# Performance work log

Hardware: AMD Instinct MI355X
Metric: run time of the kernel (lower is better)

Reference implementation:

```python
import jax, jax.numpy as jnp
import numpy as np

WSCALE = 0.05  # keep qk logits in a stable range for softmax

def setup_inputs() -> dict:
    key = jax.random.key(0)
    ks = jax.random.split(key, 7)
    B, C, H, W = 8, 256, 64, 64
    d = C // 8
    x = jax.random.normal(ks[0], (B, C, H, W), dtype=jnp.float32)
    Wq = jax.random.normal(ks[1], (d, C), dtype=jnp.float32) * WSCALE
    Wk = jax.random.normal(ks[2], (d, C), dtype=jnp.float32) * WSCALE
    Wv = jax.random.normal(ks[3], (C, C), dtype=jnp.float32) * WSCALE
    bq = jnp.zeros((d,), jnp.float32)
    bk = jnp.zeros((d,), jnp.float32)
    bv = jnp.zeros((C,), jnp.float32)
    return {"x": x, "Wq": Wq, "bq": bq, "Wk": Wk, "bk": bk, "Wv": Wv, "bv": bv}

def reference(x, Wq, bq, Wk, bk, Wv, bv):
    B, C, H, W = x.shape
    N = H * W
    xf = x.reshape(B, C, N)                                  # [B,C,N]
    # 1x1 convs == per-pixel linear projections
    q = jnp.einsum('dc,bcn->bdn', Wq, xf) + bq[None, :, None]  # [B,d,N]
    k = jnp.einsum('dc,bcn->bdn', Wk, xf) + bk[None, :, None]  # [B,d,N]
    v = jnp.einsum('ec,bcn->ben', Wv, xf) + bv[None, :, None]  # [B,C,N]
    # attn[b,i,j] = q_i . k_j ; softmax over j (keys)
    attn = jax.nn.softmax(jnp.einsum('bdi,bdj->bij', q, k), axis=-1)  # [B,N,N]
    # out[b,c,i] = sum_j v[b,c,j] * attn[b,i,j]
    out = jnp.einsum('bcj,bij->bci', v, attn)                # [B,C,N]
    return out.reshape(B, C, H, W)
```

## Files before the change

kernel.cpp:

```cpp
#include <hip/hip_runtime.h>
#include <math.h>

#define NB 8
#define NC 256
#define ND 32
#define NN 4096
#define NM 320
#define LOG2E 1.44269504088896f
#define XSTR 264

typedef short short8 __attribute__((ext_vector_type(8)));
typedef float f32x4 __attribute__((ext_vector_type(4)));

#define LDS_BARRIER() asm volatile("s_waitcnt lgkmcnt(0)\ns_barrier" ::: "memory")

__device__ __forceinline__ unsigned int f2bf_u(float f) {
    return (__float_as_uint(f) + 0x8000u) >> 16;
}
__device__ __forceinline__ unsigned short f2bf(float f) {
    return (unsigned short)f2bf_u(f);
}

__global__ __launch_bounds__(256) void repack_kernel(
    const float* __restrict__ Wq, const float* __restrict__ bq,
    const float* __restrict__ Wk, const float* __restrict__ bk,
    const float* __restrict__ Wv, const float* __restrict__ bv,
    unsigned short* __restrict__ wp, float* __restrict__ bias)
{
    const int T    = blockIdx.x * 256 + threadIdx.x;
    const int j    = T & 7;
    const int lane = (T >> 3) & 63;
    const int ks   = (T >> 9) & 7;
    const int mt   = T >> 12;
    const int m = mt * 16 + (lane & 15);
    const int k = ks * 32 + ((lane >> 4) << 3) + j;
    float wv;
    if (m < 32)       wv = Wq[m * NC + k] * LOG2E;
    else if (m < 64)  wv = Wk[(m - 32) * NC + k];
    else              wv = Wv[(m - 64) * NC + k];
    wp[T] = f2bf(wv);
    if (T < NM) {
        float bb;
        if (T < 32)      bb = bq[T] * LOG2E;
        else if (T < 64) bb = bk[T - 32];
        else             bb = bv[T - 64];
        bias[T] = bb;
    }
}

__global__ __launch_bounds__(256, 4) void proj_kernel(
    const float* __restrict__ x,
    const unsigned short* __restrict__ wp,
    const float* __restrict__ bias,
    unsigned short* __restrict__ q_ws,
    unsigned short* __restrict__ k_ws,
    unsigned short* __restrict__ v_ws)
{
    __shared__ __align__(16) unsigned short xs[32 * XSTR];

    const int b  = blockIdx.x >> 7;
    const int n0 = (blockIdx.x & 127) << 5;
    const int t  = threadIdx.x;

    {
        const int n  = t & 31;
        const int cg = t >> 5;
        const float* xb = x + (size_t)b * NC * NN + n0 + n;
        #pragma unroll
        for (int it = 0; it < 8; ++it) {
            const int c = 32 * it + 4 * cg;
            const float x0 = xb[(size_t)(c + 0) * NN];
            const float x1 = xb[(size_t)(c + 1) * NN];
            const float x2 = xb[(size_t)(c + 2) * NN];
            const float x3 = xb[(size_t)(c + 3) * NN];
            uint2 pk;
            pk.x = (f2bf_u(x1) << 16) | f2bf_u(x0);
            pk.y = (f2bf_u(x3) << 16) | f2bf_u(x2);
            *(uint2*)(xs + n * XSTR + c) = pk;
        }
    }
    __syncthreads();

    const int w    = t >> 6;
    const int lane = t & 63;
    const int li = lane & 15;
    const int qd = lane >> 4;

    f32x4 acc[5][2];
    #pragma unroll
    for (int u = 0; u < 5; ++u) {
        const float bb = bias[(w + 4 * u) * 16 + li];
        acc[u][0] = (f32x4){bb, bb, bb, bb};
        acc[u][1] = (f32x4){bb, bb, bb, bb};
    }

    #pragma unroll
    for (int ks = 0; ks < 8; ++ks) {
        short8 af[2];
        #pragma unroll
        for (int mt = 0; mt < 2; ++mt)
            af[mt] = *(const short8*)(xs + (mt * 16 + li) * XSTR + ks * 32 + qd * 8);
        #pragma unroll
        for (int u = 0; u < 5; ++u) {
            const int ct = w + 4 * u;
            const short8 bf = *(const short8*)(wp + (size_t)((ct * 8 + ks) * 64 + lane) * 8);
            acc[u][0] = __builtin_amdgcn_mfma_f32_16x16x32_bf16(af[0], bf, acc[u][0], 0, 0, 0);
            acc[u][1] = __builtin_amdgcn_mfma_f32_16x16x32_bf16(af[1], bf, acc[u][1], 0, 0, 0);
        }
    }

    #pragma unroll
    for (int u = 0; u < 5; ++u) {
        const int ct = w + 4 * u;
        if (ct < 4) {
            unsigned short* dst = (ct < 2) ? q_ws : k_ws;
            const int d = (ct & 1) * 16 + li;
            #pragma unroll
            for (int mt = 0; mt < 2; ++mt)
                #pragma unroll
                for (int r = 0; r < 4; ++r) {
                    const int n = n0 + mt * 16 + 4 * qd + r;
                    dst[((size_t)b * NN + n) * ND + d] = f2bf(acc[u][mt][r]);
                }
        } else {
            const int cv = (ct - 4) * 16 + li;
            #pragma unroll
            for (int mt = 0; mt < 2; ++mt) {
                const int n = n0 + mt * 16 + 4 * qd;
                uint2 pk;
                pk.x = (f2bf_u(acc[u][mt][1]) << 16) | f2bf_u(acc[u][mt][0]);
                pk.y = (f2bf_u(acc[u][mt][3]) << 16) | f2bf_u(acc[u][mt][2]);
                *(uint2*)(v_ws + ((size_t)b * NC + cv) * NN + n) = pk;
            }
        }
    }
}

__global__ __launch_bounds__(256, 2) void attn_kernel(
    const unsigned short* __restrict__ q_ws,
    const unsigned short* __restrict__ k_ws,
    const unsigned short* __restrict__ v_ws,
    float* __restrict__ out)
{
    __shared__ __align__(16) unsigned short Pb[2][4][16 * 72];
    __shared__ float lred[4][16];

    const int b  = blockIdx.x & 7;
    const int i0 = (blockIdx.x >> 3) * 64;
    const int w    = threadIdx.x >> 6;
    const int lane = threadIdx.x & 63;
    const int li = lane & 15;
    const int qd = lane >> 4;
    const int sw = w;
    const int c0 = 64 * w;

    const short8 qf = *(const short8*)(q_ws + ((size_t)b * NN + i0 + 16 * sw + li) * ND + qd * 8);
    const unsigned short* kb = k_ws + ((size_t)b * NN + li) * ND + qd * 8;
    const unsigned short* vb = v_ws + ((size_t)b * NC + c0 + li) * NN + qd * 8;

    unsigned short* PA = &Pb[0][0][0];
    unsigned short* PB = &Pb[1][0][0];

    f32x4 o[4][4];
    #pragma unroll
    for (int sb = 0; sb < 4; ++sb)
        #pragma unroll
        for (int ct = 0; ct < 4; ++ct)
            o[sb][ct] = (f32x4){0.f, 0.f, 0.f, 0.f};
    float l_loc = 0.f;
    const f32x4 z4 = {0.f, 0.f, 0.f, 0.f};

    short8 kA[4], kB[4], vA[4][2], vB[4][2];

    auto LKF = [&](int j0, short8 (&kf)[4]) {
        #pragma unroll
        for (int tt = 0; tt < 4; ++tt)
            kf[tt] = *(const short8*)(kb + (size_t)(j0 + 16 * tt) * ND);
    };
    auto LVF = [&](int j0, short8 (&vf)[4][2]) {
        #pragma unroll
        for (int t = 0; t < 4; ++t) {
            const unsigned short* vt = vb + (size_t)(16 * t) * NN;
            vf[t][0] = *(const short8*)(vt + j0);
            vf[t][1] = *(const short8*)(vt + j0 + 32);
        }
    };
    auto DOS = [&](short8 (&kf)[4], unsigned short* P) {
        unsigned short* Pw = P + sw * (16 * 72) + li * 72 + 4 * qd;
        #pragma unroll
        for (int tt = 0; tt < 4; ++tt) {
            const f32x4 s = __builtin_amdgcn_mfma_f32_16x16x32_bf16(kf[tt], qf, z4, 0, 0, 0);
            const float p0 = __builtin_amdgcn_exp2f(s[0]);
            const float p1 = __builtin_amdgcn_exp2f(s[1]);
            const float p2 = __builtin_amdgcn_exp2f(s[2]);
            const float p3 = __builtin_amdgcn_exp2f(s[3]);
            l_loc += (p0 + p1) + (p2 + p3);
            const unsigned u0 = __float_as_uint(p0) + 0x8000u;
            const unsigned u1 = __float_as_uint(p1) + 0x8000u;
            const unsigned u2 = __float_as_uint(p2) + 0x8000u;
            const unsigned u3 = __float_as_uint(p3) + 0x8000u;
            uint2 pk;
            pk.x = __builtin_amdgcn_perm(u1, u0, 0x07060302u);
            pk.y = __builtin_amdgcn_perm(u3, u2, 0x07060302u);
            *(uint2*)(Pw + 16 * tt) = pk;
        }
    };
    auto DOPV = [&](const unsigned short* P, short8 (&vf)[4][2]) {
        #pragma unroll
        for (int sb = 0; sb < 4; ++sb) {
            const unsigned short* Pr = P + sb * (16 * 72) + li * 72 + qd * 8;
            const short8 pf0 = *(const short8*)(Pr);
            const short8 pf1 = *(const short8*)(Pr + 32);
            #pragma unroll
            for (int ct = 0; ct < 4; ++ct) {
                o[sb][ct] = __builtin_amdgcn_mfma_f32_16x16x32_bf16(vf[ct][0], pf0, o[sb][ct], 0, 0, 0);
                o[sb][ct] = __builtin_amdgcn_mfma_f32_16x16x32_bf16(vf[ct][1], pf1, o[sb][ct], 0, 0, 0);
            }
        }
    };

    LKF(0, kA); LVF(0, vA);
    DOS(kA, PA);
    LKF(64, kB);
    LDS_BARRIER();

    int j = 0;
    #pragma unroll 1
    for (int it = 0; it < 31; ++it) {
        LVF(j + 64, vB);
        DOS(kB, PB);
        DOPV(PA, vA);
        LKF(j + 128, kA);
        LDS_BARRIER();
        LVF(j + 128, vA);
        DOS(kA, PA);
        DOPV(PB, vB);
        LKF(j + 192, kB);
        LDS_BARRIER();
        j += 128;
    }
    LVF(4032, vB);
    DOS(kB, PB);
    DOPV(PA, vA);
    LDS_BARRIER();
    DOPV(PB, vB);

    l_loc += __shfl_xor(l_loc, 16, 64);
    l_loc += __shfl_xor(l_loc, 32, 64);
    if (lane < 16) lred[w][li] = l_loc;
    __syncthreads();
    float linv[4];
    #pragma unroll
    for (int sb = 0; sb < 4; ++sb)
        linv[sb] = 1.0f / lred[sb][li];

    #pragma unroll
    for (int sb = 0; sb < 4; ++sb)
        #pragma unroll
        for (int ct = 0; ct < 4; ++ct) {
            const int c = c0 + ct * 16 + qd * 4;
            float* op = out + ((size_t)b * NC + c) * NN + i0 + 16 * sb + li;
            #pragma unroll
            for (int r = 0; r < 4; ++r)
                op[(size_t)r * NN] = o[sb][ct][r] * linv[sb];
        }
}

extern "C" void kernel_launch(void* const* d_in, const int* in_sizes, int n_in,
                              void* d_out, int out_size, void* d_ws, size_t ws_size,
                              hipStream_t stream) {
    const float* x  = (const float*)d_in[0];
    const float* Wq = (const float*)d_in[1];
    const float* bq = (const float*)d_in[2];
    const float* Wk = (const float*)d_in[3];
    const float* bk = (const float*)d_in[4];
    const float* Wv = (const float*)d_in[5];
    const float* bv = (const float*)d_in[6];
    float* out = (float*)d_out;

    unsigned short* q_ws = (unsigned short*)d_ws;
    unsigned short* k_ws = q_ws + (size_t)NB * NN * ND;
    unsigned short* v_ws = k_ws + (size_t)NB * NN * ND;
    unsigned short* wp   = v_ws + (size_t)NB * NC * NN;
    float*          bias = (float*)(wp + (size_t)NM * NC);

    repack_kernel<<<NM * NC / 256, 256, 0, stream>>>(Wq, bq, Wk, bk, Wv, bv, wp, bias);
    proj_kernel<<<NB * (NN / 32), 256, 0, stream>>>(x, wp, bias, q_ws, k_ws, v_ws);
    attn_kernel<<<NB * (NN / 64), 256, 0, stream>>>(q_ws, k_ws, v_ws, out);
}
```

Baseline: 252.3 us.

## Quad-buffer P tiles in LDS to halve barriers in attention loop

Grows the shared P (softmax probability) buffer from two to four tiles and reorganises the pipelined loop so each barrier covers two key/value blocks instead of one. Loop trip count halves (15 iterations of 256 keys) and the prologue/epilogue are rewritten to match. The goal is to cut workgroup barrier stalls and give more slack between the score and PV MFMA phases. It doubles the P LDS footprint, which may lower occupancy, and it changes the register live ranges.

Result: no change. 247.4 us (-1.9%).

```diff
diff --git a/kernel.cpp b/kernel.cpp
--- a/kernel.cpp
+++ b/kernel.cpp
@@ -142,7 +142,7 @@
     const unsigned short* __restrict__ v_ws,
     float* __restrict__ out)
 {
-    __shared__ __align__(16) unsigned short Pb[2][4][16 * 72];
+    __shared__ __align__(16) unsigned short Pb[4][4][16 * 72];
     __shared__ float lred[4][16];
 
     const int b  = blockIdx.x & 7;
@@ -158,8 +158,10 @@
     const unsigned short* kb = k_ws + ((size_t)b * NN + li) * ND + qd * 8;
     const unsigned short* vb = v_ws + ((size_t)b * NC + c0 + li) * NN + qd * 8;
 
-    unsigned short* PA = &Pb[0][0][0];
-    unsigned short* PB = &Pb[1][0][0];
+    unsigned short* Pq0 = &Pb[0][0][0];
+    unsigned short* Pq1 = &Pb[1][0][0];
+    unsigned short* Pq2 = &Pb[2][0][0];
+    unsigned short* Pq3 = &Pb[3][0][0];
 
     f32x4 o[4][4];
     #pragma unroll
@@ -219,31 +221,46 @@
         }
     };
 
-    LKF(0, kA); LVF(0, vA);
-    DOS(kA, PA);
-    LKF(64, kB);
+    LKF(0, kA); LKF(64, kB); LVF(0, vA);
+    DOS(kA, Pq0);
+    DOS(kB, Pq1);
+    LKF(128, kA);
     LDS_BARRIER();
 
     int j = 0;
     #pragma unroll 1
-    for (int it = 0; it < 31; ++it) {
+    for (int it = 0; it < 15; ++it) {
         LVF(j + 64, vB);
-        DOS(kB, PB);
-        DOPV(PA, vA);
-        LKF(j + 128, kA);
+        DOPV(Pq0, vA);
+        DOS(kA, Pq2);
+        LKF(j + 192, kB);
+        LVF(j + 128, vA);
+        DOPV(Pq1, vB);
+        DOS(kB, Pq3);
+        LKF(j + 256, kA);
         LDS_BARRIER();
-        LVF(j + 128, vA);
-        DOS(kA, PA);
-        DOPV(PB, vB);
-        LKF(j + 192, kB);
+        LVF(j + 192, vB);
+        DOPV(Pq2, vA);
+        DOS(kA, Pq0);
+        LKF(j + 320, kB);
+        LVF(j + 256, vA);
+        DOPV(Pq3, vB);
+        DOS(kB, Pq1);
+        LKF(j + 384, kA);
         LDS_BARRIER();
-        j += 128;
-    }
+        j += 256;
+    }
+    LVF(3904, vB);
+    DOPV(Pq0, vA);
+    DOS(kA, Pq2);
+    LKF(4032, kB);
+    LVF(3968, vA);
+    DOPV(Pq1, vB);
+    DOS(kB, Pq3);
+    LDS_BARRIER();
     LVF(4032, vB);
-    DOS(kB, PB);
-    DOPV(PA, vA);
-    LDS_BARRIER();
-    DOPV(PB, vB);
+    DOPV(Pq2, vA);
+    DOPV(Pq3, vB);
 
     l_loc += __shfl_xor(l_loc, 16, 64);
     l_loc += __shfl_xor(l_loc, 32, 64);
```

## Keep attention probabilities in registers and drop LDS exchange between waves

Applied to the files above, without the earlier changes.

Each wave now computes the scores for all four 16-row query sub-blocks itself instead of sharing them through LDS. The bf16 probabilities feed straight from the QK MFMA output layout into 16x16x16 PV MFMAs, so the LDS buffers and per-chunk barriers go away. This costs 4x redundant QK MFMAs and exp2 work per wave, plus smaller 8-byte V loads and twice as many PV MFMA instructions. Sched barriers pin the order of loads and compute.

New measurement: 588.0 us. 133% more time.

```diff
diff --git a/kernel.cpp b/kernel.cpp
--- a/kernel.cpp
+++ b/kernel.cpp
@@ -10,9 +10,8 @@
 #define XSTR 264
 
 typedef short short8 __attribute__((ext_vector_type(8)));
+typedef short short4v __attribute__((ext_vector_type(4)));
 typedef float f32x4 __attribute__((ext_vector_type(4)));
-
-#define LDS_BARRIER() asm volatile("s_waitcnt lgkmcnt(0)\ns_barrier" ::: "memory")
 
 __device__ __forceinline__ unsigned int f2bf_u(float f) {
     return (__float_as_uint(f) + 0x8000u) >> 16;
@@ -142,24 +141,24 @@
     const unsigned short* __restrict__ v_ws,
     float* __restrict__ out)
 {
-    __shared__ __align__(16) unsigned short Pb[2][4][16 * 72];
-    __shared__ float lred[4][16];
-
     const int b  = blockIdx.x & 7;
     const int i0 = (blockIdx.x >> 3) * 64;
     const int w    = threadIdx.x >> 6;
     const int lane = threadIdx.x & 63;
     const int li = lane & 15;
     const int qd = lane >> 4;
-    const int sw = w;
     const int c0 = 64 * w;
 
-    const short8 qf = *(const short8*)(q_ws + ((size_t)b * NN + i0 + 16 * sw + li) * ND + qd * 8);
+    short8 qf[4];
+    #pragma unroll
+    for (int sb = 0; sb < 4; ++sb)
+        qf[sb] = *(const short8*)(q_ws + ((size_t)b * NN + i0 + 16 * sb + li) * ND + qd * 8);
+
     const unsigned short* kb = k_ws + ((size_t)b * NN + li) * ND + qd * 8;
-    const unsigned short* vb = v_ws + ((size_t)b * NC + c0 + li) * NN + qd * 8;
-
-    unsigned short* PA = &Pb[0][0][0];
-    unsigned short* PB = &Pb[1][0][0];
+    const unsigned short* vrow[4];
+    #pragma unroll
+    for (int ct = 0; ct < 4; ++ct)
+        vrow[ct] = v_ws + ((size_t)b * NC + c0 + 16 * ct + li) * NN + qd * 4;
 
     f32x4 o[4][4];
     #pragma unroll
@@ -167,103 +166,88 @@
         #pragma unroll
         for (int ct = 0; ct < 4; ++ct)
             o[sb][ct] = (f32x4){0.f, 0.f, 0.f, 0.f};
-    float l_loc = 0.f;
+    float l_loc[4] = {0.f, 0.f, 0.f, 0.f};
     const f32x4 z4 = {0.f, 0.f, 0.f, 0.f};
 
-    short8 kA[4], kB[4], vA[4][2], vB[4][2];
-
-    auto LKF = [&](int j0, short8 (&kf)[4]) {
-        #pragma unroll
-        for (int tt = 0; tt < 4; ++tt)
-            kf[tt] = *(const short8*)(kb + (size_t)(j0 + 16 * tt) * ND);
+    short8 kA[4], kB[4];
+    uint2  vA[4][4], vB[4][4];
+
+    auto LK = [&](int j0, short8 (&kf)[4]) {
+        #pragma unroll
+        for (int jt = 0; jt < 4; ++jt)
+            kf[jt] = *(const short8*)(kb + (size_t)(j0 + 16 * jt) * ND);
     };
-    auto LVF = [&](int j0, short8 (&vf)[4][2]) {
-        #pragma unroll
-        for (int t = 0; t < 4; ++t) {
-            const unsigned short* vt = vb + (size_t)(16 * t) * NN;
-            vf[t][0] = *(const short8*)(vt + j0);
-            vf[t][1] = *(const short8*)(vt + j0 + 32);
-        }
+    auto LV = [&](int j0, uint2 (&vf)[4][4]) {
+        #pragma unroll
+        for (int ct = 0; ct < 4; ++ct)
+            #pragma unroll
+            for (int jt = 0; jt < 4; ++jt)
+                vf[ct][jt] = *(const uint2*)(vrow[ct] + j0 + 16 * jt);
     };
-    auto DOS = [&](short8 (&kf)[4], unsigned short* P) {
-        unsigned short* Pw = P + sw * (16 * 72) + li * 72 + 4 * qd;
-        #pragma unroll
-        for (int tt = 0; tt < 4; ++tt) {
-            const f32x4 s = __builtin_amdgcn_mfma_f32_16x16x32_bf16(kf[tt], qf, z4, 0, 0, 0);
-            const float p0 = __builtin_amdgcn_exp2f(s[0]);
-            const float p1 = __builtin_amdgcn_exp2f(s[1]);
-            const float p2 = __builtin_amdgcn_exp2f(s[2]);
-            const float p3 = __builtin_amdgcn_exp2f(s[3]);
-            l_loc += (p0 + p1) + (p2 + p3);
-            const unsigned u0 = __float_as_uint(p0) + 0x8000u;
-            const unsigned u1 = __float_as_uint(p1) + 0x8000u;
-            const unsigned u2 = __float_as_uint(p2) + 0x8000u;
-            const unsigned u3 = __float_as_uint(p3) + 0x8000u;
-            uint2 pk;
-            pk.x = __builtin_amdgcn_perm(u1, u0, 0x07060302u);
-            pk.y = __builtin_amdgcn_perm(u3, u2, 0x07060302u);
-            *(uint2*)(Pw + 16 * tt) = pk;
+    auto CHUNK = [&](short8 (&kf)[4], uint2 (&vf)[4][4]) {
+        #pragma unroll
+        for (int sb = 0; sb < 4; ++sb) {
+            uint2 pk[4];
+            #pragma unroll
+            for (int jt = 0; jt < 4; ++jt) {
+                const f32x4 s = __builtin_amdgcn_mfma_f32_16x16x32_bf16(kf[jt], qf[sb], z4, 0, 0, 0);
+                const float p0 = __builtin_amdgcn_exp2f(s[0]);
+                const float p1 = __builtin_amdgcn_exp2f(s[1]);
+                const float p2 = __builtin_amdgcn_exp2f(s[2]);
+                const float p3 = __builtin_amdgcn_exp2f(s[3]);
+                l_loc[sb] += (p0 + p1) + (p2 + p3);
+                const unsigned u0 = __float_as_uint(p0) + 0x8000u;
+                const unsigned u1 = __float_as_uint(p1) + 0x8000u;
+                const unsigned u2 = __float_as_uint(p2) + 0x8000u;
+                const unsigned u3 = __float_as_uint(p3) + 0x8000u;
+                pk[jt].x = __builtin_amdgcn_perm(u1, u0, 0x07060302u);
+                pk[jt].y = __builtin_amdgcn_perm(u3, u2, 0x07060302u);
+            }
+            #pragma unroll
+            for (int ct = 0; ct < 4; ++ct)
+                #pragma unroll
+                for (int jt = 0; jt < 4; ++jt)
+                    o[sb][ct] = __builtin_amdgcn_mfma_f32_16x16x16bf16_1k(
+                        __builtin_bit_cast(short4v, vf[ct][jt]),
+                        __builtin_bit_cast(short4v, pk[jt]),
+                        o[sb][ct], 0, 0, 0);
         }
     };
-    auto DOPV = [&](const unsigned short* P, short8 (&vf)[4][2]) {
-        #pragma unroll
-        for (int sb = 0; sb < 4; ++sb) {
-            const unsigned short* Pr = P + sb * (16 * 72) + li * 72 + qd * 8;
-            const short8 pf0 = *(const short8*)(Pr);
-            const short8 pf1 = *(const short8*)(Pr + 32);
-            #pragma unroll
-            for (int ct = 0; ct < 4; ++ct) {
-                o[sb][ct] = __builtin_amdgcn_mfma_f32_16x16x32_bf16(vf[ct][0], pf0, o[sb][ct], 0, 0, 0);
-                o[sb][ct] = __builtin_amdgcn_mfma_f32_16x16x32_bf16(vf[ct][1], pf1, o[sb][ct], 0, 0, 0);
-            }
-        }
-    };
-
-    LKF(0, kA); LVF(0, vA);
-    DOS(kA, PA);
-    LKF(64, kB);
-    LDS_BARRIER();
-
-    int j = 0;
+
+    LK(0, kA); LV(0, vA);
     #pragma unroll 1
     for (int it = 0; it < 31; ++it) {
-        LVF(j + 64, vB);
-        DOS(kB, PB);
-        DOPV(PA, vA);
-        LKF(j + 128, kA);
-        LDS_BARRIER();
-        LVF(j + 128, vA);
-        DOS(kA, PA);
-        DOPV(PB, vB);
-        LKF(j + 192, kB);
-        LDS_BARRIER();
-        j += 128;
-    }
-    LVF(4032, vB);
-    DOS(kB, PB);
-    DOPV(PA, vA);
-    LDS_BARRIER();
-    DOPV(PB, vB);
-
-    l_loc += __shfl_xor(l_loc, 16, 64);
-    l_loc += __shfl_xor(l_loc, 32, 64);
-    if (lane < 16) lred[w][li] = l_loc;
-    __syncthreads();
-    float linv[4];
-    #pragma unroll
-    for (int sb = 0; sb < 4; ++sb)
-        linv[sb] = 1.0f / lred[sb][li];
-
-    #pragma unroll
-    for (int sb = 0; sb < 4; ++sb)
+        const int j = it * 128;
+        LK(j + 64, kB); LV(j + 64, vB);
+        __builtin_amdgcn_sched_barrier(0);
+        CHUNK(kA, vA);
+        LK(j + 128, kA); LV(j + 128, vA);
+        __builtin_amdgcn_sched_barrier(0);
+        CHUNK(kB, vB);
+    }
+    LK(4032, kB); LV(4032, vB);
+    __builtin_amdgcn_sched_barrier(0);
+    CHUNK(kA, vA);
+    CHUNK(kB, vB);
+
+    #pragma unroll
+    for (int sb = 0; sb < 4; ++sb) {
+        l_loc[sb] += __shfl_xor(l_loc[sb], 16, 64);
+        l_loc[sb] += __shfl_xor(l_loc[sb], 32, 64);
+    }
+
+    #pragma unroll
+    for (int sb = 0; sb < 4; ++sb) {
+        const float linv = 1.0f / l_loc[sb];
         #pragma unroll
         for (int ct = 0; ct < 4; ++ct) {
             const int c = c0 + ct * 16 + qd * 4;
             float* op = out + ((size_t)b * NC + c) * NN + i0 + 16 * sb + li;
             #pragma unroll
             for (int r = 0; r < 4; ++r)
-                op[(size_t)r * NN] = o[sb][ct][r] * linv[sb];
-        }
+                op[(size_t)r * NN] = o[sb][ct][r] * linv;
+        }
+    }
 }
 
 extern "C" void kernel_launch(void* const* d_in, const int* in_sizes, int n_in,
```
